# Optimization experiments

Hardware: AMD Instinct MI355X
Metric: run time of the kernel (lower is better)

## Reference

```python
import jax, jax.numpy as jnp
import numpy as np

N_NODES = 50000
N_GRAPHS = 512
HID = 128
IN = 128
SLOPE = 0.2  # LeakyReLU negative slope (PyG default)


def _gatv2(x, src, dst, Wl, bl, Wr, br, att, bias, n):
    # PyG GATv2Conv, 1 head: xl used for source/messages, xr for targets
    xl = x @ Wl + bl          # [N, H]
    xr = x @ Wr + br          # [N, H]
    # per-edge score: att . LeakyReLU(xl[j] + xr[i])
    e = jax.nn.leaky_relu(xl[src] + xr[dst], SLOPE) @ att  # [E]
    # softmax grouped by destination node (self loops guarantee nonempty groups)
    m = jax.ops.segment_max(e, dst, num_segments=n)
    p = jnp.exp(e - m[dst])
    s = jax.ops.segment_sum(p, dst, num_segments=n)
    alpha = p / s[dst]                                      # [E]
    out = jax.ops.segment_sum(alpha[:, None] * xl[src], dst, num_segments=n)
    return out + bias


def setup_inputs() -> dict:
    key = jax.random.key(0)
    ks = jax.random.split(key, 24)
    x = jax.random.normal(ks[0], (N_NODES, IN), jnp.float32)
    edge_index = jax.random.randint(ks[1], (2, 1600000), 0, N_NODES, jnp.int64)
    batch = jnp.sort(jax.random.randint(ks[2], (N_NODES,), 0, N_GRAPHS, jnp.int64))

    def lin(k, fi, fo):
        k1, k2 = jax.random.split(k)
        sc = 1.0 / np.sqrt(fi)
        return (jax.random.uniform(k1, (fi, fo), jnp.float32, -sc, sc),
                jax.random.uniform(k2, (fo,), jnp.float32, -sc, sc))

    d = {"x": x, "edge_index": edge_index, "batch": batch}
    dims = [(IN, HID), (HID, HID), (HID, HID)]
    for i, (fi, fo) in enumerate(dims, 1):
        Wl, bl = lin(ks[3 * i], fi, fo)
        Wr, br = lin(ks[3 * i + 1], fi, fo)
        d[f"Wl{i}"], d[f"bl{i}"] = Wl, bl
        d[f"Wr{i}"], d[f"br{i}"] = Wr, br
        d[f"att{i}"] = jax.random.normal(ks[3 * i + 2], (fo,), jnp.float32) / np.sqrt(fo)
        d[f"bias{i}"] = jnp.zeros((fo,), jnp.float32)
    d["W4"], d["b4"] = lin(ks[15], HID, 128)
    d["W5"], d["b5"] = lin(ks[16], 128, 64)
    d["W6"], d["b6"] = lin(ks[17], 64, 2)
    return d


def reference(x, edge_index, batch,
              Wl1, bl1, Wr1, br1, att1, bias1,
              Wl2, bl2, Wr2, br2, att2, bias2,
              Wl3, bl3, Wr3, br3, att3, bias3,
              W4, b4, W5, b5, W6, b6):
    n = x.shape[0]
    loop = jnp.arange(n, dtype=edge_index.dtype)
    src = jnp.concatenate([edge_index[0], loop])  # add_self_loops=True
    dst = jnp.concatenate([edge_index[1], loop])

    h = jax.nn.relu(_gatv2(x, src, dst, Wl1, bl1, Wr1, br1, att1, bias1, n))
    h = jax.nn.relu(_gatv2(h, src, dst, Wl2, bl2, Wr2, br2, att2, bias2, n))
    h = _gatv2(h, src, dst, Wl3, bl3, Wr3, br3, att3, bias3, n)

    # global_mean_pool over graph ids
    sums = jax.ops.segment_sum(h, batch, num_segments=N_GRAPHS)
    cnts = jax.ops.segment_sum(jnp.ones((n,), h.dtype), batch, num_segments=N_GRAPHS)
    g = sums / jnp.maximum(cnts, 1.0)[:, None]

    # dropout is identity in eval mode; MLP head
    g = jax.nn.sigmoid(g @ W4 + b4)
    g = jax.nn.sigmoid(g @ W5 + b5)
    return g @ W6 + b6
```

## Files before the change

kernel.cpp:

```cpp
#include <hip/hip_runtime.h>
#include <hip/hip_bf16.h>
#include <math.h>

#define BK_SHIFT 7
#define BK_NODES 128

typedef _Float16 h2 __attribute__((ext_vector_type(2)));
typedef _Float16 f16x8 __attribute__((ext_vector_type(8)));
typedef float f32x4 __attribute__((ext_vector_type(4)));

__device__ __forceinline__ h2 u2h(unsigned u){ return __builtin_bit_cast(h2, u); }

__device__ __forceinline__ int dev_lower_bound(const int* __restrict__ a, int n, int v){
  int lo = 0, hi = n;
  while (lo < hi){ int mid = (lo + hi) >> 1; if (a[mid] < v) lo = mid + 1; else hi = mid; }
  return lo;
}

__global__ __launch_bounds__(256) void p1_bucket_count(const int* __restrict__ edst,
    int* __restrict__ bktTotal, int nE, int K){
  __shared__ int cnt[512];
  for (int k = threadIdx.x; k < K; k += 256) cnt[k] = 0;
  __syncthreads();
  int i = (blockIdx.x * 256 + threadIdx.x) * 8;
  if (i + 7 < nE){
    int4 a = *(const int4*)(edst + i);
    int4 b = *(const int4*)(edst + i + 4);
    atomicAdd(&cnt[a.x >> BK_SHIFT], 1); atomicAdd(&cnt[a.y >> BK_SHIFT], 1);
    atomicAdd(&cnt[a.z >> BK_SHIFT], 1); atomicAdd(&cnt[a.w >> BK_SHIFT], 1);
    atomicAdd(&cnt[b.x >> BK_SHIFT], 1); atomicAdd(&cnt[b.y >> BK_SHIFT], 1);
    atomicAdd(&cnt[b.z >> BK_SHIFT], 1); atomicAdd(&cnt[b.w >> BK_SHIFT], 1);
  } else {
    for (int j = i; j < nE; ++j) atomicAdd(&cnt[edst[j] >> BK_SHIFT], 1);
  }
  __syncthreads();
  for (int k = threadIdx.x; k < K; k += 256)
    if (cnt[k]) atomicAdd(&bktTotal[k], cnt[k]);
}

__global__ __launch_bounds__(512) void p2_scan(const int* __restrict__ bktTotal,
    int* __restrict__ bktBase, int* __restrict__ bktCur,
    int* __restrict__ row_off, int K, int n, int nE){
  __shared__ int sh[512];
  int t = threadIdx.x;
  int v = (t < K) ? bktTotal[t] : 0;
  sh[t] = v;
  __syncthreads();
  for (int off = 1; off < 512; off <<= 1){
    int u = (t >= off) ? sh[t - off] : 0;
    __syncthreads();
    sh[t] += u;
    __syncthreads();
  }
  if (t < K){
    int excl = sh[t] - v;
    bktBase[t] = excl;
    bktCur[t]  = excl;
  }
  if (t == 0){
    bktBase[K] = nE;
    row_off[n] = nE + n;
  }
}

__global__ __launch_bounds__(256) void p3_partition(const int* __restrict__ esrc,
    const int* __restrict__ edst, int* __restrict__ bktCur,
    int2* __restrict__ ebuf, int nE, int K){
  __shared__ int cnt[512];
  __shared__ int base[512];
  for (int k = threadIdx.x; k < K; k += 256) cnt[k] = 0;
  __syncthreads();
  const int i0 = (blockIdx.x * 256 + threadIdx.x) * 8;
  const int i1 = min(i0 + 8, nE);
  int bkt[8];
  int sv[8], dv[8];
  int cnt_local = i1 - i0;
  for (int j = 0; j < cnt_local; ++j){
    sv[j] = esrc[i0 + j];
    dv[j] = edst[i0 + j];
    bkt[j] = dv[j] >> BK_SHIFT;
    atomicAdd(&cnt[bkt[j]], 1);
  }
  __syncthreads();
  for (int k = threadIdx.x; k < K; k += 256){
    int c = cnt[k];
    base[k] = c ? atomicAdd(&bktCur[k], c) : 0;
  }
  __syncthreads();
  for (int k = threadIdx.x; k < K; k += 256) cnt[k] = 0;
  __syncthreads();
  for (int j = 0; j < cnt_local; ++j){
    int r = atomicAdd(&cnt[bkt[j]], 1);
    ebuf[base[bkt[j]] + r] = make_int2(sv[j], dv[j]);
  }
}

__global__ __launch_bounds__(256) void p4_build(const int2* __restrict__ ebuf,
    const int* __restrict__ bktBase, int* __restrict__ row_off,
    int* __restrict__ csr_src, int n){
  const int b = blockIdx.x;
  const int node0 = b << BK_SHIFT;
  const int nNodes = min(BK_NODES, n - node0);
  const int tid = threadIdx.x;
  __shared__ int ldeg[BK_NODES];
  __shared__ int lcur[BK_NODES];
  __shared__ int sc[BK_NODES];
  const int e0 = bktBase[b];
  const int e1 = bktBase[b + 1];
  if (tid < BK_NODES) ldeg[tid] = 0;
  __syncthreads();
  for (int i = e0 + tid; i < e1; i += 256)
    atomicAdd(&ldeg[ebuf[i].y - node0], 1);
  __syncthreads();
  if (tid < BK_NODES) sc[tid] = (tid < nNodes) ? (ldeg[tid] + 1) : 0;
  __syncthreads();
  for (int off = 1; off < BK_NODES; off <<= 1){
    int u = 0;
    if (tid < BK_NODES && tid >= off) u = sc[tid - off];
    __syncthreads();
    if (tid < BK_NODES) sc[tid] += u;
    __syncthreads();
  }
  if (tid < nNodes){
    const int csr0 = e0 + node0;
    int ro = csr0 + sc[tid] - (ldeg[tid] + 1);
    row_off[node0 + tid] = ro;
    lcur[tid] = ro;
  }
  __syncthreads();
  for (int i = e0 + tid; i < e1; i += 256){
    int2 e = ebuf[i];
    int p = atomicAdd(&lcur[e.y - node0], 1);
    csr_src[p] = e.x;
  }
  __syncthreads();
  if (tid < nNodes)
    csr_src[lcur[tid]] = node0 + tid;
}

__global__ __launch_bounds__(256) void deg_hist(const int* __restrict__ row_off,
    int* __restrict__ dbins, int n){
  __shared__ int cnt[256];
  cnt[threadIdx.x] = 0;
  __syncthreads();
  int i = blockIdx.x * 256 + threadIdx.x;
  if (i < n){
    int deg = row_off[i + 1] - row_off[i];
    atomicAdd(&cnt[min(deg, 255)], 1);
  }
  __syncthreads();
  if (cnt[threadIdx.x]) atomicAdd(&dbins[threadIdx.x], cnt[threadIdx.x]);
}

__global__ __launch_bounds__(256) void deg_scan(const int* __restrict__ dbins,
    int* __restrict__ dcur){
  __shared__ int sh[256];
  int t = threadIdx.x;
  int v = dbins[t];
  sh[t] = v;
  __syncthreads();
  for (int off = 1; off < 256; off <<= 1){
    int u = (t >= off) ? sh[t - off] : 0;
    __syncthreads();
    sh[t] += u;
    __syncthreads();
  }
  dcur[t] = sh[t] - v;
}

__global__ __launch_bounds__(256) void deg_scatter(const int* __restrict__ row_off,
    int* __restrict__ dcur, int* __restrict__ order, int n){
  __shared__ int cnt[256];
  __shared__ int base[256];
  cnt[threadIdx.x] = 0;
  __syncthreads();
  int i = blockIdx.x * 256 + threadIdx.x;
  int bin = 0, r = 0;
  if (i < n){
    int deg = row_off[i + 1] - row_off[i];
    bin = min(deg, 255);
    r = atomicAdd(&cnt[bin], 1);
  }
  __syncthreads();
  base[threadIdx.x] = cnt[threadIdx.x] ? atomicAdd(&dcur[threadIdx.x], cnt[threadIdx.x]) : 0;
  __syncthreads();
  if (i < n) order[base[bin] + r] = i;
}

__global__ __launch_bounds__(256) void prep_w_kernel(
    const float* __restrict__ W0, const float* __restrict__ W1,
    const float* __restrict__ W2, const float* __restrict__ W3,
    const float* __restrict__ W4m, const float* __restrict__ W5m,
    unsigned short* __restrict__ Wt16)
{
  const float* Ws[6] = {W0, W1, W2, W3, W4m, W5m};
  const int mat = blockIdx.x >> 3;
  const int chunk = blockIdx.x & 7;
  const float* W = Ws[mat];
  unsigned short* o = Wt16 + mat * 16384;
  #pragma unroll
  for (int e = 0; e < 8; ++e){
    int i = chunk * 2048 + e * 256 + threadIdx.x;
    int k = i >> 7, col = i & 127;
    _Float16 h = (_Float16)W[i];
    o[col * 128 + k] = __builtin_bit_cast(unsigned short, h);
  }
}

template<bool F16IN>
__global__ __launch_bounds__(256) void gemm_mfma_kernel(
    const void* __restrict__ Xv,
    const unsigned short* __restrict__ WtL,
    const float* __restrict__ bl, const float* __restrict__ br,
    unsigned short* __restrict__ xl16, unsigned short* __restrict__ xr16, int n)
{
  const int mat = blockIdx.y;
  const unsigned short* Wt = WtL + mat * 16384;
  const float* bias = mat ? br : bl;
  unsigned short* out = mat ? xr16 : xl16;
  const int w   = threadIdx.x >> 6;
  const int l   = threadIdx.x & 63;
  const int l15 = l & 15;
  const int kq  = l >> 4;
  const int rowbase = blockIdx.x * 128 + w * 32;

  f16x8 a[2][4];
  #pragma unroll
  for (int rt = 0; rt < 2; ++rt){
    const int r = rowbase + rt * 16 + l15;
    const bool ok = r < n;
    const int rc = min(r, n - 1);
    #pragma unroll
    for (int ks = 0; ks < 4; ++ks){
      if (F16IN){
        const unsigned short* src = (const unsigned short*)Xv + (size_t)rc * 128 + kq * 8 + ks * 32;
        f16x8 v = ok ? *(const f16x8*)src : (f16x8){0,0,0,0,0,0,0,0};
        a[rt][ks] = v;
      } else {
        const float* src = (const float*)Xv + (size_t)rc * 128 + kq * 8 + ks * 32;
        float4 f0 = ok ? *(const float4*)(src)     : make_float4(0.f,0.f,0.f,0.f);
        float4 f1 = ok ? *(const float4*)(src + 4) : make_float4(0.f,0.f,0.f,0.f);
        f16x8 v;
        v[0] = (_Float16)f0.x; v[1] = (_Float16)f0.y;
        v[2] = (_Float16)f0.z; v[3] = (_Float16)f0.w;
        v[4] = (_Float16)f1.x; v[5] = (_Float16)f1.y;
        v[6] = (_Float16)f1.z; v[7] = (_Float16)f1.w;
        a[rt][ks] = v;
      }
    }
  }

  f32x4 acc[2][8];
  #pragma unroll
  for (int rt = 0; rt < 2; ++rt)
    #pragma unroll
    for (int ct = 0; ct < 8; ++ct)
      acc[rt][ct] = (f32x4){0.f, 0.f, 0.f, 0.f};

  #pragma unroll
  for (int ks = 0; ks < 4; ++ks){
    #pragma unroll
    for (int ct = 0; ct < 8; ++ct){
      f16x8 b = *(const f16x8*)(Wt + (size_t)(ct * 16 + l15) * 128 + ks * 32 + kq * 8);
      acc[0][ct] = __builtin_amdgcn_mfma_f32_16x16x32_f16(a[0][ks], b, acc[0][ct], 0, 0, 0);
      acc[1][ct] = __builtin_amdgcn_mfma_f32_16x16x32_f16(a[1][ks], b, acc[1][ct], 0, 0, 0);
    }
  }

  #pragma unroll
  for (int ct = 0; ct < 8; ++ct){
    const float bv = bias[ct * 16 + l15];
    #pragma unroll
    for (int rt = 0; rt < 2; ++rt){
      #pragma unroll
      for (int rg = 0; rg < 4; ++rg){
        const int r = rowbase + rt * 16 + kq * 4 + rg;
        if (r < n){
          _Float16 h = (_Float16)(acc[rt][ct][rg] + bv);
          out[(size_t)r * 128 + ct * 16 + l15] = __builtin_bit_cast(unsigned short, h);
        }
      }
    }
  }
}

__global__ __launch_bounds__(256) void edge_attn_kernel(
    const unsigned short* __restrict__ xl16, const unsigned short* __restrict__ xr16,
    const int* __restrict__ row_off, const int* __restrict__ csr_src,
    const int* __restrict__ order,
    const float* __restrict__ att, const float* __restrict__ bias,
    unsigned short* __restrict__ out16, int n, int do_relu)
{
  const int gid = (blockIdx.x * blockDim.x + threadIdx.x) >> 4;
  const int node = order[min(gid, n - 1)];
  const int lane16 = threadIdx.x & 15;
  const int f8 = lane16 * 8;

  const uint4 xru = *(const uint4*)(xr16 + (size_t)node * 128 + f8);
  const h2 xr0 = u2h(xru.x), xr1 = u2h(xru.y), xr2 = u2h(xru.z), xr3 = u2h(xru.w);
  const float4 aA = *(const float4*)(att + f8);
  const float4 aB = *(const float4*)(att + f8 + 4);
  const h2 at0 = {(_Float16)aA.x, (_Float16)aA.y};
  const h2 at1 = {(_Float16)aA.z, (_Float16)aA.w};
  const h2 at2 = {(_Float16)aB.x, (_Float16)aB.y};
  const h2 at3 = {(_Float16)aB.z, (_Float16)aB.w};
  const h2 k02 = {(_Float16)0.2f, (_Float16)0.2f};

  const int base = row_off[node];
  const int deg  = row_off[node + 1] - base;
  int dmax = max(deg, __shfl_xor(deg, 16));
  dmax = max(dmax, __shfl_xor(dmax, 32));

  auto part = [&](uint4 xp) -> float {
    h2 u0 = u2h(xp.x) + xr0;
    h2 u1 = u2h(xp.y) + xr1;
    h2 u2 = u2h(xp.z) + xr2;
    h2 u3 = u2h(xp.w) + xr3;
    u0 = __builtin_elementwise_max(u0, u0 * k02);
    u1 = __builtin_elementwise_max(u1, u1 * k02);
    u2 = __builtin_elementwise_max(u2, u2 * k02);
    u3 = __builtin_elementwise_max(u3, u3 * k02);
    float ps = __builtin_amdgcn_fdot2(u0, at0, 0.f, false);
    ps = __builtin_amdgcn_fdot2(u1, at1, ps, false);
    ps = __builtin_amdgcn_fdot2(u2, at2, ps, false);
    ps = __builtin_amdgcn_fdot2(u3, at3, ps, false);
    return ps;
  };

  uint4 xp = *(const uint4*)(xl16 + (size_t)csr_src[base] * 128 + f8);
  float p = part(xp);
  p += __shfl_xor(p, 1); p += __shfl_xor(p, 2);
  p += __shfl_xor(p, 4); p += __shfl_xor(p, 8);
  float m = p, Mrun = p, s = 1.f;
  float a0 = (float)u2h(xp.x).x, a1 = (float)u2h(xp.x).y;
  float a2 = (float)u2h(xp.y).x, a3 = (float)u2h(xp.y).y;
  float a4 = (float)u2h(xp.z).x, a5 = (float)u2h(xp.z).y;
  float a6 = (float)u2h(xp.w).x, a7 = (float)u2h(xp.w).y;

  for (int it = 1; it < dmax; it += 4){
    const int c0 = min(it,     deg - 1);
    const int c1 = min(it + 1, deg - 1);
    const int c2 = min(it + 2, deg - 1);
    const int c3 = min(it + 3, deg - 1);
    const int s0 = csr_src[base + c0];
    const int s1 = csr_src[base + c1];
    const int s2 = csr_src[base + c2];
    const int s3 = csr_src[base + c3];
    const uint4 xA = *(const uint4*)(xl16 + (size_t)s0 * 128 + f8);
    const uint4 xB = *(const uint4*)(xl16 + (size_t)s1 * 128 + f8);
    const uint4 xC = *(const uint4*)(xl16 + (size_t)s2 * 128 + f8);
    const uint4 xD = *(const uint4*)(xl16 + (size_t)s3 * 128 + f8);
    float pA = part(xA), pB = part(xB), pC = part(xC), pD = part(xD);
    #pragma unroll
    for (int off = 1; off < 16; off <<= 1){
      pA += __shfl_xor(pA, off);
      pB += __shfl_xor(pB, off);
      pC += __shfl_xor(pC, off);
      pD += __shfl_xor(pD, off);
    }
    const bool vA = it < deg, vB = it + 1 < deg, vC = it + 2 < deg, vD = it + 3 < deg;
    float fA = vA ? pA : -3.0e38f;
    float fB = vB ? pB : -3.0e38f;
    float fC = vC ? pC : -3.0e38f;
    float fD = vD ? pD : -3.0e38f;
    Mrun = fmaxf(Mrun, fmaxf(fmaxf(fA, fB), fmaxf(fC, fD)));
    if (__any(Mrun > m + 8.f)){
      float sc = __expf(m - Mrun);
      s *= sc;
      a0 *= sc; a1 *= sc; a2 *= sc; a3 *= sc;
      a4 *= sc; a5 *= sc; a6 *= sc; a7 *= sc;
      m = Mrun;
    }
    float qA = vA ? __expf(pA - m) : 0.f;
    float qB = vB ? __expf(pB - m) : 0.f;
    float qC = vC ? __expf(pC - m) : 0.f;
    float qD = vD ? __expf(pD - m) : 0.f;
    s += (qA + qB) + (qC + qD);
    h2 w;
    w = u2h(xA.x); a0 = fmaf(qA, (float)w.x, a0); a1 = fmaf(qA, (float)w.y, a1);
    w = u2h(xA.y); a2 = fmaf(qA, (float)w.x, a2); a3 = fmaf(qA, (float)w.y, a3);
    w = u2h(xA.z); a4 = fmaf(qA, (float)w.x, a4); a5 = fmaf(qA, (float)w.y, a5);
    w = u2h(xA.w); a6 = fmaf(qA, (float)w.x, a6); a7 = fmaf(qA, (float)w.y, a7);
    w = u2h(xB.x); a0 = fmaf(qB, (float)w.x, a0); a1 = fmaf(qB, (float)w.y, a1);
    w = u2h(xB.y); a2 = fmaf(qB, (float)w.x, a2); a3 = fmaf(qB, (float)w.y, a3);
    w = u2h(xB.z); a4 = fmaf(qB, (float)w.x, a4); a5 = fmaf(qB, (float)w.y, a5);
    w = u2h(xB.w); a6 = fmaf(qB, (float)w.x, a6); a7 = fmaf(qB, (float)w.y, a7);
    w = u2h(xC.x); a0 = fmaf(qC, (float)w.x, a0); a1 = fmaf(qC, (float)w.y, a1);
    w = u2h(xC.y); a2 = fmaf(qC, (float)w.x, a2); a3 = fmaf(qC, (float)w.y, a3);
    w = u2h(xC.z); a4 = fmaf(qC, (float)w.x, a4); a5 = fmaf(qC, (float)w.y, a5);
    w = u2h(xC.w); a6 = fmaf(qC, (float)w.x, a6); a7 = fmaf(qC, (float)w.y, a7);
    w = u2h(xD.x); a0 = fmaf(qD, (float)w.x, a0); a1 = fmaf(qD, (float)w.y, a1);
    w = u2h(xD.y); a2 = fmaf(qD, (float)w.x, a2); a3 = fmaf(qD, (float)w.y, a3);
    w = u2h(xD.z); a4 = fmaf(qD, (float)w.x, a4); a5 = fmaf(qD, (float)w.y, a5);
    w = u2h(xD.w); a6 = fmaf(qD, (float)w.x, a6); a7 = fmaf(qD, (float)w.y, a7);
  }

  if (gid < n){
    const float inv = 1.0f / s;
    const float4 bA = *(const float4*)(bias + f8);
    const float4 bB = *(const float4*)(bias + f8 + 4);
    float o0 = fmaf(a0, inv, bA.x), o1 = fmaf(a1, inv, bA.y);
    float o2 = fmaf(a2, inv, bA.z), o3 = fmaf(a3, inv, bA.w);
    float o4 = fmaf(a4, inv, bB.x), o5 = fmaf(a5, inv, bB.y);
    float o6 = fmaf(a6, inv, bB.z), o7 = fmaf(a7, inv, bB.w);
    if (do_relu){
      o0 = fmaxf(o0, 0.f); o1 = fmaxf(o1, 0.f); o2 = fmaxf(o2, 0.f); o3 = fmaxf(o3, 0.f);
      o4 = fmaxf(o4, 0.f); o5 = fmaxf(o5, 0.f); o6 = fmaxf(o6, 0.f); o7 = fmaxf(o7, 0.f);
    }
    ushort4 wlo, whi;
    wlo.x = __builtin_bit_cast(unsigned short, (_Float16)o0);
    wlo.y = __builtin_bit_cast(unsigned short, (_Float16)o1);
    wlo.z = __builtin_bit_cast(unsigned short, (_Float16)o2);
    wlo.w = __builtin_bit_cast(unsigned short, (_Float16)o3);
    whi.x = __builtin_bit_cast(unsigned short, (_Float16)o4);
    whi.y = __builtin_bit_cast(unsigned short, (_Float16)o5);
    whi.z = __builtin_bit_cast(unsigned short, (_Float16)o6);
    whi.w = __builtin_bit_cast(unsigned short, (_Float16)o7);
    *(ushort4*)(out16 + (size_t)node * 128 + f8)     = wlo;
    *(ushort4*)(out16 + (size_t)node * 128 + f8 + 4) = whi;
  }
}

__global__ __launch_bounds__(128) void pool_mlp_kernel(
    const unsigned short* __restrict__ h, const int* __restrict__ batch, int n,
    const float* __restrict__ W4, const float* __restrict__ b4,
    const float* __restrict__ W5, const float* __restrict__ b5,
    const float* __restrict__ W6, const float* __restrict__ b6,
    float* __restrict__ out)
{
  int g = blockIdx.x;
  int t = threadIdx.x;
  __shared__ float gf[128];
  __shared__ float h1[128];
  __shared__ float h2s[64];
  int lo = dev_lower_bound(batch, n, g);
  int hi = dev_lower_bound(batch, n, g + 1);
  float ssum = 0.f;
  for (int i = lo; i < hi; ++i){
    _Float16 hv = __builtin_bit_cast(_Float16, h[(size_t)i * 128 + t]);
    ssum += (float)hv;
  }
  float cnt = (float)(hi - lo);
  gf[t] = ssum / fmaxf(cnt, 1.0f);
  __syncthreads();
  float a = b4[t];
  for (int k = 0; k < 128; ++k) a = fmaf(gf[k], W4[k * 128 + t], a);
  h1[t] = 1.0f / (1.0f + __expf(-a));
  __syncthreads();
  if (t < 64){
    float a5 = b5[t];
    for (int k = 0; k < 128; ++k) a5 = fmaf(h1[k], W5[k * 64 + t], a5);
    h2s[t] = 1.0f / (1.0f + __expf(-a5));
  }
  __syncthreads();
  if (t < 2){
    float a6 = b6[t];
    for (int k = 0; k < 64; ++k) a6 = fmaf(h2s[k], W6[k * 2 + t], a6);
    out[g * 2 + t] = a6;
  }
}

extern "C" void kernel_launch(void* const* d_in, const int* in_sizes, int n_in,
                              void* d_out, int out_size, void* d_ws, size_t ws_size,
                              hipStream_t stream)
{
  const float* x          = (const float*)d_in[0];
  const int*   edge_index = (const int*)d_in[1];
  const int*   batch      = (const int*)d_in[2];
  const int n  = in_sizes[0] / 128;
  const int nE = in_sizes[1] / 2;
  const int* esrc = edge_index;
  const int* edst = edge_index + nE;
  const int n_graphs = out_size / 2;
  const int K = (n + BK_NODES - 1) >> BK_SHIFT;

  const float *Wl[3], *bl[3], *Wr[3], *br[3], *att[3], *bias[3];
  for (int l = 0; l < 3; ++l){
    Wl[l]   = (const float*)d_in[3 + 6 * l + 0];
    bl[l]   = (const float*)d_in[3 + 6 * l + 1];
    Wr[l]   = (const float*)d_in[3 + 6 * l + 2];
    br[l]   = (const float*)d_in[3 + 6 * l + 3];
    att[l]  = (const float*)d_in[3 + 6 * l + 4];
    bias[l] = (const float*)d_in[3 + 6 * l + 5];
  }
  const float* W4 = (const float*)d_in[21]; const float* b4 = (const float*)d_in[22];
  const float* W5 = (const float*)d_in[23]; const float* b5 = (const float*)d_in[24];
  const float* W6 = (const float*)d_in[25]; const float* b6 = (const float*)d_in[26];

  char* ws = (char*)d_ws;
  size_t off = 0;
  auto alloc = [&](size_t bytes) -> void* {
    void* p = ws + off;
    off = (off + bytes + 255) & ~(size_t)255;
    return p;
  };
  int*   row_off  = (int*)  alloc((size_t)(n + 1) * sizeof(int));
  int*   bktTotal = (int*)  alloc(512 * sizeof(int));
  int*   bktBase  = (int*)  alloc(513 * sizeof(int));
  int*   bktCur   = (int*)  alloc(512 * sizeof(int));
  int*   dbins    = (int*)  alloc(256 * sizeof(int));
  int*   dcur     = (int*)  alloc(256 * sizeof(int));
  int*   order    = (int*)  alloc((size_t)n * sizeof(int));
  int*   csr_src  = (int*)  alloc((size_t)(nE + n) * sizeof(int));
  int2*  ebuf     = (int2*) alloc((size_t)nE * sizeof(int2));
  unsigned short* xlb16 = (unsigned short*)alloc((size_t)n * 128 * sizeof(unsigned short));
  unsigned short* xrb16 = (unsigned short*)alloc((size_t)n * 128 * sizeof(unsigned short));
  unsigned short* Wt16  = (unsigned short*)alloc(6 * 16384 * sizeof(unsigned short));
  unsigned short* hC16  = (unsigned short*)alloc((size_t)n * 128 * sizeof(unsigned short));
  (void)ws_size; (void)n_in;

  prep_w_kernel<<<48, 256, 0, stream>>>(Wl[0], Wr[0], Wl[1], Wr[1], Wl[2], Wr[2], Wt16);

  hipMemsetAsync(bktTotal, 0, 512 * sizeof(int), stream);
  hipMemsetAsync(dbins, 0, 256 * sizeof(int), stream);
  const int eblocks = (nE + 2048 - 1) / 2048;
  p1_bucket_count<<<eblocks, 256, 0, stream>>>(edst, bktTotal, nE, K);
  p2_scan<<<1, 512, 0, stream>>>(bktTotal, bktBase, bktCur, row_off, K, n, nE);
  p3_partition<<<eblocks, 256, 0, stream>>>(esrc, edst, bktCur, ebuf, nE, K);
  p4_build<<<K, 256, 0, stream>>>(ebuf, bktBase, row_off, csr_src, n);

  const int nblocks = (n + 255) / 256;
  deg_hist<<<nblocks, 256, 0, stream>>>(row_off, dbins, n);
  deg_scan<<<1, 256, 0, stream>>>(dbins, dcur);
  deg_scatter<<<nblocks, 256, 0, stream>>>(row_off, dcur, order, n);

  const int gemm_tiles = (n + 127) / 128;
  const int attn_blocks = (int)(((size_t)n * 16 + 255) / 256);

  gemm_mfma_kernel<false><<<dim3(gemm_tiles, 2), 256, 0, stream>>>(x, Wt16 + 0 * 32768,
                                                            bl[0], br[0], xlb16, xrb16, n);
  edge_attn_kernel<<<attn_blocks, 256, 0, stream>>>(xlb16, xrb16, row_off, csr_src, order,
                                                    att[0], bias[0], hC16, n, 1);
  gemm_mfma_kernel<true><<<dim3(gemm_tiles, 2), 256, 0, stream>>>(hC16, Wt16 + 1 * 32768,
                                                            bl[1], br[1], xlb16, xrb16, n);
  edge_attn_kernel<<<attn_blocks, 256, 0, stream>>>(xlb16, xrb16, row_off, csr_src, order,
                                                    att[1], bias[1], hC16, n, 1);
  gemm_mfma_kernel<true><<<dim3(gemm_tiles, 2), 256, 0, stream>>>(hC16, Wt16 + 2 * 32768,
                                                            bl[2], br[2], xlb16, xrb16, n);
  edge_attn_kernel<<<attn_blocks, 256, 0, stream>>>(xlb16, xrb16, row_off, csr_src, order,
                                                    att[2], bias[2], hC16, n, 0);

  pool_mlp_kernel<<<n_graphs, 128, 0, stream>>>(hC16, batch, n, W4, b4, W5, b5, W6, b6,
                                                (float*)d_out);
}
```

Baseline: 431.8 us.

## Pack edge buffer into 32-bit words and prefetch next neighbor batch in aggregation

The bucket partition now stores each edge as a single 32-bit word, the source id shifted left with the low 7 bits of the destination, instead of an int2. This halves the write and read traffic of the edge buffer in the CSR build. The attention aggregation loop is software-pipelined so the next four neighbor rows are loaded while the current four are scored and accumulated, hiding gather latency. The cost is more live vector registers for the prefetched rows, and the packing requires source ids below 2^25.

```diff
diff --git a/kernel.cpp b/kernel.cpp
--- a/kernel.cpp
+++ b/kernel.cpp
@@ -1,5 +1,4 @@
 #include <hip/hip_runtime.h>
-#include <hip/hip_bf16.h>
 #include <math.h>
 
 #define BK_SHIFT 7
@@ -65,7 +64,7 @@
 
 __global__ __launch_bounds__(256) void p3_partition(const int* __restrict__ esrc,
     const int* __restrict__ edst, int* __restrict__ bktCur,
-    int2* __restrict__ ebuf, int nE, int K){
+    unsigned* __restrict__ ebuf, int nE, int K){
   __shared__ int cnt[512];
   __shared__ int base[512];
   for (int k = threadIdx.x; k < K; k += 256) cnt[k] = 0;
@@ -73,12 +72,13 @@
   const int i0 = (blockIdx.x * 256 + threadIdx.x) * 8;
   const int i1 = min(i0 + 8, nE);
   int bkt[8];
-  int sv[8], dv[8];
+  unsigned pk[8];
   int cnt_local = i1 - i0;
   for (int j = 0; j < cnt_local; ++j){
-    sv[j] = esrc[i0 + j];
-    dv[j] = edst[i0 + j];
-    bkt[j] = dv[j] >> BK_SHIFT;
+    int sv = esrc[i0 + j];
+    int dv = edst[i0 + j];
+    bkt[j] = dv >> BK_SHIFT;
+    pk[j] = ((unsigned)sv << BK_SHIFT) | (unsigned)(dv & (BK_NODES - 1));
     atomicAdd(&cnt[bkt[j]], 1);
   }
   __syncthreads();
@@ -91,11 +91,11 @@
   __syncthreads();
   for (int j = 0; j < cnt_local; ++j){
     int r = atomicAdd(&cnt[bkt[j]], 1);
-    ebuf[base[bkt[j]] + r] = make_int2(sv[j], dv[j]);
-  }
-}
-
-__global__ __launch_bounds__(256) void p4_build(const int2* __restrict__ ebuf,
+    ebuf[base[bkt[j]] + r] = pk[j];
+  }
+}
+
+__global__ __launch_bounds__(256) void p4_build(const unsigned* __restrict__ ebuf,
     const int* __restrict__ bktBase, int* __restrict__ row_off,
     int* __restrict__ csr_src, int n){
   const int b = blockIdx.x;
@@ -110,7 +110,7 @@
   if (tid < BK_NODES) ldeg[tid] = 0;
   __syncthreads();
   for (int i = e0 + tid; i < e1; i += 256)
-    atomicAdd(&ldeg[ebuf[i].y - node0], 1);
+    atomicAdd(&ldeg[ebuf[i] & (BK_NODES - 1)], 1);
   __syncthreads();
   if (tid < BK_NODES) sc[tid] = (tid < nNodes) ? (ldeg[tid] + 1) : 0;
   __syncthreads();
@@ -129,9 +129,9 @@
   }
   __syncthreads();
   for (int i = e0 + tid; i < e1; i += 256){
-    int2 e = ebuf[i];
-    int p = atomicAdd(&lcur[e.y - node0], 1);
-    csr_src[p] = e.x;
+    unsigned e = ebuf[i];
+    int p = atomicAdd(&lcur[e & (BK_NODES - 1)], 1);
+    csr_src[p] = (int)(e >> BK_SHIFT);
   }
   __syncthreads();
   if (tid < nNodes)
@@ -337,19 +337,31 @@
   float a4 = (float)u2h(xp.z).x, a5 = (float)u2h(xp.z).y;
   float a6 = (float)u2h(xp.w).x, a7 = (float)u2h(xp.w).y;
 
-  for (int it = 1; it < dmax; it += 4){
+  int it = 1;
+  uint4 xA = {}, xB = {}, xC = {}, xD = {};
+  if (it < dmax){
     const int c0 = min(it,     deg - 1);
     const int c1 = min(it + 1, deg - 1);
     const int c2 = min(it + 2, deg - 1);
     const int c3 = min(it + 3, deg - 1);
-    const int s0 = csr_src[base + c0];
-    const int s1 = csr_src[base + c1];
-    const int s2 = csr_src[base + c2];
-    const int s3 = csr_src[base + c3];
-    const uint4 xA = *(const uint4*)(xl16 + (size_t)s0 * 128 + f8);
-    const uint4 xB = *(const uint4*)(xl16 + (size_t)s1 * 128 + f8);
-    const uint4 xC = *(const uint4*)(xl16 + (size_t)s2 * 128 + f8);
-    const uint4 xD = *(const uint4*)(xl16 + (size_t)s3 * 128 + f8);
+    xA = *(const uint4*)(xl16 + (size_t)csr_src[base + c0] * 128 + f8);
+    xB = *(const uint4*)(xl16 + (size_t)csr_src[base + c1] * 128 + f8);
+    xC = *(const uint4*)(xl16 + (size_t)csr_src[base + c2] * 128 + f8);
+    xD = *(const uint4*)(xl16 + (size_t)csr_src[base + c3] * 128 + f8);
+  }
+  while (it < dmax){
+    const int itn = it + 4;
+    uint4 yA = {}, yB = {}, yC = {}, yD = {};
+    if (itn < dmax){
+      const int c0 = min(itn,     deg - 1);
+      const int c1 = min(itn + 1, deg - 1);
+      const int c2 = min(itn + 2, deg - 1);
+      const int c3 = min(itn + 3, deg - 1);
+      yA = *(const uint4*)(xl16 + (size_t)csr_src[base + c0] * 128 + f8);
+      yB = *(const uint4*)(xl16 + (size_t)csr_src[base + c1] * 128 + f8);
+      yC = *(const uint4*)(xl16 + (size_t)csr_src[base + c2] * 128 + f8);
+      yD = *(const uint4*)(xl16 + (size_t)csr_src[base + c3] * 128 + f8);
+    }
     float pA = part(xA), pB = part(xB), pC = part(xC), pD = part(xD);
     #pragma unroll
     for (int off = 1; off < 16; off <<= 1){
@@ -393,6 +405,8 @@
     w = u2h(xD.y); a2 = fmaf(qD, (float)w.x, a2); a3 = fmaf(qD, (float)w.y, a3);
     w = u2h(xD.z); a4 = fmaf(qD, (float)w.x, a4); a5 = fmaf(qD, (float)w.y, a5);
     w = u2h(xD.w); a6 = fmaf(qD, (float)w.x, a6); a7 = fmaf(qD, (float)w.y, a7);
+    it = itn;
+    xA = yA; xB = yB; xC = yC; xD = yD;
   }
 
   if (gid < n){
@@ -502,7 +516,7 @@
   int*   dcur     = (int*)  alloc(256 * sizeof(int));
   int*   order    = (int*)  alloc((size_t)n * sizeof(int));
   int*   csr_src  = (int*)  alloc((size_t)(nE + n) * sizeof(int));
-  int2*  ebuf     = (int2*) alloc((size_t)nE * sizeof(int2));
+  unsigned* ebuf  = (unsigned*)alloc((size_t)nE * sizeof(unsigned));
   unsigned short* xlb16 = (unsigned short*)alloc((size_t)n * 128 * sizeof(unsigned short));
   unsigned short* xrb16 = (unsigned short*)alloc((size_t)n * 128 * sizeof(unsigned short));
   unsigned short* Wt16  = (unsigned short*)alloc(6 * 16384 * sizeof(unsigned short));
```

Result: no change. 435.9 us (+1.0%).

## Fuse CSR preprocessing kernels, pack edges, sort neighbors in LDS

Applied to the files above, without the earlier changes.

Folds the weight transpose into the bucket-count kernel and the degree histogram into the CSR build kernel, and merges the memsets into one. Edges are packed into a single 32-bit word (source shifted, local destination in the low bits), which halves partition traffic. The CSR build now stages each bucket's neighbour list in a shared buffer and insertion-sorts each node's sources before writing them out contiguously, so later gathers hit memory in a more orderly way. The risks are the fixed shared buffer size, which assumes no bucket holds more than about 5K edges, and the serial per-thread insertion sort on high-degree nodes.

```diff
diff --git a/kernel.cpp b/kernel.cpp
--- a/kernel.cpp
+++ b/kernel.cpp
@@ -1,9 +1,9 @@
 #include <hip/hip_runtime.h>
-#include <hip/hip_bf16.h>
 #include <math.h>
 
 #define BK_SHIFT 7
 #define BK_NODES 128
+#define P4_BUF 4992
 
 typedef _Float16 h2 __attribute__((ext_vector_type(2)));
 typedef _Float16 f16x8 __attribute__((ext_vector_type(8)));
@@ -17,12 +17,33 @@
   return lo;
 }
 
-__global__ __launch_bounds__(256) void p1_bucket_count(const int* __restrict__ edst,
-    int* __restrict__ bktTotal, int nE, int K){
+__global__ __launch_bounds__(256) void p1_prep_kernel(
+    const int* __restrict__ edst, int* __restrict__ bktTotal, int nE, int K,
+    const float* __restrict__ W0, const float* __restrict__ W1,
+    const float* __restrict__ W2, const float* __restrict__ W3,
+    const float* __restrict__ W4m, const float* __restrict__ W5m,
+    unsigned short* __restrict__ Wt16)
+{
   __shared__ int cnt[512];
+  if (blockIdx.x < 48){
+    const float* Ws[6] = {W0, W1, W2, W3, W4m, W5m};
+    const int mat = blockIdx.x >> 3;
+    const int chunk = blockIdx.x & 7;
+    const float* W = Ws[mat];
+    unsigned short* o = Wt16 + mat * 16384;
+    #pragma unroll
+    for (int e = 0; e < 8; ++e){
+      int i = chunk * 2048 + e * 256 + threadIdx.x;
+      int k = i >> 7, col = i & 127;
+      _Float16 h = (_Float16)W[i];
+      o[col * 128 + k] = __builtin_bit_cast(unsigned short, h);
+    }
+    return;
+  }
+  const int bx = blockIdx.x - 48;
   for (int k = threadIdx.x; k < K; k += 256) cnt[k] = 0;
   __syncthreads();
-  int i = (blockIdx.x * 256 + threadIdx.x) * 8;
+  int i = (bx * 256 + threadIdx.x) * 8;
   if (i + 7 < nE){
     int4 a = *(const int4*)(edst + i);
     int4 b = *(const int4*)(edst + i + 4);
@@ -65,7 +86,7 @@
 
 __global__ __launch_bounds__(256) void p3_partition(const int* __restrict__ esrc,
     const int* __restrict__ edst, int* __restrict__ bktCur,
-    int2* __restrict__ ebuf, int nE, int K){
+    unsigned* __restrict__ ebuf, int nE, int K){
   __shared__ int cnt[512];
   __shared__ int base[512];
   for (int k = threadIdx.x; k < K; k += 256) cnt[k] = 0;
@@ -73,12 +94,13 @@
   const int i0 = (blockIdx.x * 256 + threadIdx.x) * 8;
   const int i1 = min(i0 + 8, nE);
   int bkt[8];
-  int sv[8], dv[8];
+  unsigned pk[8];
   int cnt_local = i1 - i0;
   for (int j = 0; j < cnt_local; ++j){
-    sv[j] = esrc[i0 + j];
-    dv[j] = edst[i0 + j];
-    bkt[j] = dv[j] >> BK_SHIFT;
+    int sv = esrc[i0 + j];
+    int dv = edst[i0 + j];
+    bkt[j] = dv >> BK_SHIFT;
+    pk[j] = ((unsigned)sv << BK_SHIFT) | (unsigned)(dv & (BK_NODES - 1));
     atomicAdd(&cnt[bkt[j]], 1);
   }
   __syncthreads();
@@ -91,26 +113,31 @@
   __syncthreads();
   for (int j = 0; j < cnt_local; ++j){
     int r = atomicAdd(&cnt[bkt[j]], 1);
-    ebuf[base[bkt[j]] + r] = make_int2(sv[j], dv[j]);
-  }
-}
-
-__global__ __launch_bounds__(256) void p4_build(const int2* __restrict__ ebuf,
+    ebuf[base[bkt[j]] + r] = pk[j];
+  }
+}
+
+__global__ __launch_bounds__(256) void p4_build(const unsigned* __restrict__ ebuf,
     const int* __restrict__ bktBase, int* __restrict__ row_off,
-    int* __restrict__ csr_src, int n){
+    int* __restrict__ csr_src, int* __restrict__ dbins, int n){
   const int b = blockIdx.x;
   const int node0 = b << BK_SHIFT;
   const int nNodes = min(BK_NODES, n - node0);
   const int tid = threadIdx.x;
   __shared__ int ldeg[BK_NODES];
+  __shared__ int lro[BK_NODES];
   __shared__ int lcur[BK_NODES];
   __shared__ int sc[BK_NODES];
+  __shared__ int dh[256];
+  __shared__ int buf[P4_BUF];
   const int e0 = bktBase[b];
   const int e1 = bktBase[b + 1];
+  const int total = (e1 - e0) + nNodes;
   if (tid < BK_NODES) ldeg[tid] = 0;
+  dh[tid] = 0;
   __syncthreads();
   for (int i = e0 + tid; i < e1; i += 256)
-    atomicAdd(&ldeg[ebuf[i].y - node0], 1);
+    atomicAdd(&ldeg[ebuf[i] & (BK_NODES - 1)], 1);
   __syncthreads();
   if (tid < BK_NODES) sc[tid] = (tid < nNodes) ? (ldeg[tid] + 1) : 0;
   __syncthreads();
@@ -122,34 +149,36 @@
     __syncthreads();
   }
   if (tid < nNodes){
-    const int csr0 = e0 + node0;
-    int ro = csr0 + sc[tid] - (ldeg[tid] + 1);
-    row_off[node0 + tid] = ro;
-    lcur[tid] = ro;
+    int start = sc[tid] - (ldeg[tid] + 1);
+    lro[tid]  = start;
+    lcur[tid] = start;
+    row_off[node0 + tid] = e0 + node0 + start;
+    atomicAdd(&dh[min(ldeg[tid] + 1, 255)], 1);
   }
   __syncthreads();
   for (int i = e0 + tid; i < e1; i += 256){
-    int2 e = ebuf[i];
-    int p = atomicAdd(&lcur[e.y - node0], 1);
-    csr_src[p] = e.x;
-  }
-  __syncthreads();
-  if (tid < nNodes)
-    csr_src[lcur[tid]] = node0 + tid;
-}
-
-__global__ __launch_bounds__(256) void deg_hist(const int* __restrict__ row_off,
-    int* __restrict__ dbins, int n){
-  __shared__ int cnt[256];
-  cnt[threadIdx.x] = 0;
-  __syncthreads();
-  int i = blockIdx.x * 256 + threadIdx.x;
-  if (i < n){
-    int deg = row_off[i + 1] - row_off[i];
-    atomicAdd(&cnt[min(deg, 255)], 1);
-  }
-  __syncthreads();
-  if (cnt[threadIdx.x]) atomicAdd(&dbins[threadIdx.x], cnt[threadIdx.x]);
+    unsigned e = ebuf[i];
+    int p = atomicAdd(&lcur[e & (BK_NODES - 1)], 1);
+    buf[p] = (int)(e >> BK_SHIFT);
+  }
+  __syncthreads();
+  if (tid < nNodes){
+    const int st = lro[tid];
+    int len = ldeg[tid];
+    buf[st + len] = node0 + tid;
+    len += 1;
+    for (int i2 = 1; i2 < len; ++i2){
+      int v = buf[st + i2];
+      int j = i2 - 1;
+      while (j >= 0 && buf[st + j] > v){ buf[st + j + 1] = buf[st + j]; --j; }
+      buf[st + j + 1] = v;
+    }
+  }
+  __syncthreads();
+  const int g0 = e0 + node0;
+  for (int i = tid; i < total; i += 256)
+    csr_src[g0 + i] = buf[i];
+  if (dh[tid]) atomicAdd(&dbins[tid], dh[tid]);
 }
 
 __global__ __launch_bounds__(256) void deg_scan(const int* __restrict__ dbins,
@@ -185,26 +214,6 @@
   base[threadIdx.x] = cnt[threadIdx.x] ? atomicAdd(&dcur[threadIdx.x], cnt[threadIdx.x]) : 0;
   __syncthreads();
   if (i < n) order[base[bin] + r] = i;
-}
-
-__global__ __launch_bounds__(256) void prep_w_kernel(
-    const float* __restrict__ W0, const float* __restrict__ W1,
-    const float* __restrict__ W2, const float* __restrict__ W3,
-    const float* __restrict__ W4m, const float* __restrict__ W5m,
-    unsigned short* __restrict__ Wt16)
-{
-  const float* Ws[6] = {W0, W1, W2, W3, W4m, W5m};
-  const int mat = blockIdx.x >> 3;
-  const int chunk = blockIdx.x & 7;
-  const float* W = Ws[mat];
-  unsigned short* o = Wt16 + mat * 16384;
-  #pragma unroll
-  for (int e = 0; e < 8; ++e){
-    int i = chunk * 2048 + e * 256 + threadIdx.x;
-    int k = i >> 7, col = i & 127;
-    _Float16 h = (_Float16)W[i];
-    o[col * 128 + k] = __builtin_bit_cast(unsigned short, h);
-  }
 }
 
 template<bool F16IN>
@@ -495,34 +504,32 @@
     return p;
   };
   int*   row_off  = (int*)  alloc((size_t)(n + 1) * sizeof(int));
-  int*   bktTotal = (int*)  alloc(512 * sizeof(int));
-  int*   bktBase  = (int*)  alloc(513 * sizeof(int));
-  int*   bktCur   = (int*)  alloc(512 * sizeof(int));
-  int*   dbins    = (int*)  alloc(256 * sizeof(int));
-  int*   dcur     = (int*)  alloc(256 * sizeof(int));
+  int*   meta     = (int*)  alloc(2049 * sizeof(int));
+  int*   bktTotal = meta;
+  int*   bktBase  = meta + 512;
+  int*   bktCur   = meta + 1025;
+  int*   dbins    = meta + 1537;
+  int*   dcur     = meta + 1793;
   int*   order    = (int*)  alloc((size_t)n * sizeof(int));
   int*   csr_src  = (int*)  alloc((size_t)(nE + n) * sizeof(int));
-  int2*  ebuf     = (int2*) alloc((size_t)nE * sizeof(int2));
+  unsigned* ebuf  = (unsigned*)alloc((size_t)nE * sizeof(unsigned));
   unsigned short* xlb16 = (unsigned short*)alloc((size_t)n * 128 * sizeof(unsigned short));
   unsigned short* xrb16 = (unsigned short*)alloc((size_t)n * 128 * sizeof(unsigned short));
   unsigned short* Wt16  = (unsigned short*)alloc(6 * 16384 * sizeof(unsigned short));
   unsigned short* hC16  = (unsigned short*)alloc((size_t)n * 128 * sizeof(unsigned short));
   (void)ws_size; (void)n_in;
 
-  prep_w_kernel<<<48, 256, 0, stream>>>(Wl[0], Wr[0], Wl[1], Wr[1], Wl[2], Wr[2], Wt16);
-
-  hipMemsetAsync(bktTotal, 0, 512 * sizeof(int), stream);
-  hipMemsetAsync(dbins, 0, 256 * sizeof(int), stream);
+  hipMemsetAsync(meta, 0, 2049 * sizeof(int), stream);
+
   const int eblocks = (nE + 2048 - 1) / 2048;
-  p1_bucket_count<<<eblocks, 256, 0, stream>>>(edst, bktTotal, nE, K);
+  p1_prep_kernel<<<eblocks + 48, 256, 0, stream>>>(edst, bktTotal, nE, K,
+      Wl[0], Wr[0], Wl[1], Wr[1], Wl[2], Wr[2], Wt16);
   p2_scan<<<1, 512, 0, stream>>>(bktTotal, bktBase, bktCur, row_off, K, n, nE);
   p3_partition<<<eblocks, 256, 0, stream>>>(esrc, edst, bktCur, ebuf, nE, K);
-  p4_build<<<K, 256, 0, stream>>>(ebuf, bktBase, row_off, csr_src, n);
-
-  const int nblocks = (n + 255) / 256;
-  deg_hist<<<nblocks, 256, 0, stream>>>(row_off, dbins, n);
+  p4_build<<<K, 256, 0, stream>>>(ebuf, bktBase, row_off, csr_src, dbins, n);
+
   deg_scan<<<1, 256, 0, stream>>>(dbins, dcur);
-  deg_scatter<<<nblocks, 256, 0, stream>>>(row_off, dcur, order, n);
+  deg_scatter<<<(n + 255) / 256, 256, 0, stream>>>(row_off, dcur, order, n);
 
   const int gemm_tiles = (n + 127) / 128;
   const int attn_blocks = (int)(((size_t)n * 16 + 255) / 256);
```

Result: slower. 543.1 us (+25.8%).
